# Kernel optimization log

Measured on AMD Instinct MI355X. Metric: run time of the kernel, lower is better.

Reference implementation:

```python
import jax, jax.numpy as jnp
import numpy as np

VTH = 1.0
DECAY = 0.25


def setup_inputs() -> dict:
    key = jax.random.key(0)
    x = jax.random.normal(key, (32, 64, 16384), dtype=jnp.float32)
    return {"x": x}


def reference(x):
    # x: [T, B, N]; sequential leaky-integrate-fire over T with hard reset.
    def step(mem, xt):
        mem = mem * DECAY + xt
        out_s = (mem > VTH).astype(mem.dtype)
        out_bp = jnp.clip(mem, VTH - 1.0, VTH + 1.0) * 0.5  # surrogate
        # forward value = out_s (0/1), gradient flows through out_bp
        out_i = jax.lax.stop_gradient(out_s - out_bp) + out_bp
        mem = mem * (1.0 - out_i)  # reset=True branch
        return mem, out_i

    mem0 = jnp.zeros_like(x[0])
    _, out = jax.lax.scan(step, mem0, x)
    return out
```

## Files before the change

kernel.cpp:

```cpp
#include <hip/hip_runtime.h>


typedef float f32x2 __attribute__((ext_vector_type(2)));

__global__ __launch_bounds__(256) void lif_fwd_kernel(
    const f32x2* __restrict__ x, f32x2* __restrict__ out, int BN2, int T) {
    const int i = blockIdx.x * blockDim.x + threadIdx.x;
    if (i >= BN2) return;

    const f32x2* xp = x + i;
    f32x2* op = out + i;

    float mx = 0.f, my = 0.f;

    #pragma unroll 32
    for (int t = 0; t < T; ++t) {
        const f32x2 xt = xp[(size_t)t * (size_t)BN2];

        f32x2 s;
        mx = mx * 0.25f + xt.x;
        my = my * 0.25f + xt.y;

        s.x = (mx > 1.0f) ? 1.0f : 0.0f;
        s.y = (my > 1.0f) ? 1.0f : 0.0f;

        mx = (s.x != 0.0f) ? 0.0f : mx;
        my = (s.y != 0.0f) ? 0.0f : my;

        op[(size_t)t * (size_t)BN2] = s;
    }
}

extern "C" void kernel_launch(void* const* d_in, const int* in_sizes, int n_in,
                              void* d_out, int out_size, void* d_ws, size_t ws_size,
                              hipStream_t stream) {
    const float* x = (const float*)d_in[0];
    float* out = (float*)d_out;

    const int T = 32;
    const int total = in_sizes[0];
    const int BN = total / T;
    const int BN2 = BN / 2;

    const int block = 256;
    const int grid = (BN2 + block - 1) / block;

    lif_fwd_kernel<<<grid, block, 0, stream>>>(
        (const f32x2*)x, (f32x2*)out, BN2, T);
}
```

Before: 45.49 us.

## Prefetch all timesteps into registers with scalar per-thread elements

Each thread now handles one float instead of a float2 pair and loads all 32 timesteps into registers before running the sequential recurrence. Issuing every load up front is meant to expose memory-level parallelism and hide latency, and doubling the thread count raises occupancy. The occupancy hint of 8 blocks per CU and the removed bounds check assume BN divides evenly by 256. The exchange is narrower 4-byte accesses and 32 live registers per thread.

After: 51.54 us. 1.13x slower.

```diff
diff --git a/kernel.cpp b/kernel.cpp
--- a/kernel.cpp
+++ b/kernel.cpp
@@ -1,33 +1,22 @@
 #include <hip/hip_runtime.h>
 
 
-typedef float f32x2 __attribute__((ext_vector_type(2)));
+__global__ __launch_bounds__(256, 8) void lif_fwd_kernel(
+    const float* __restrict__ x, float* __restrict__ out, int BN) {
+    const size_t i = (size_t)blockIdx.x * 256 + threadIdx.x;
 
-__global__ __launch_bounds__(256) void lif_fwd_kernel(
-    const f32x2* __restrict__ x, f32x2* __restrict__ out, int BN2, int T) {
-    const int i = blockIdx.x * blockDim.x + threadIdx.x;
-    if (i >= BN2) return;
+    float xv[32];
+    #pragma unroll
+    for (int t = 0; t < 32; ++t)
+        xv[t] = x[(size_t)t * BN + i];
 
-    const f32x2* xp = x + i;
-    f32x2* op = out + i;
-
-    float mx = 0.f, my = 0.f;
-
-    #pragma unroll 32
-    for (int t = 0; t < T; ++t) {
-        const f32x2 xt = xp[(size_t)t * (size_t)BN2];
-
-        f32x2 s;
-        mx = mx * 0.25f + xt.x;
-        my = my * 0.25f + xt.y;
-
-        s.x = (mx > 1.0f) ? 1.0f : 0.0f;
-        s.y = (my > 1.0f) ? 1.0f : 0.0f;
-
-        mx = (s.x != 0.0f) ? 0.0f : mx;
-        my = (s.y != 0.0f) ? 0.0f : my;
-
-        op[(size_t)t * (size_t)BN2] = s;
+    float mem = 0.f;
+    #pragma unroll
+    for (int t = 0; t < 32; ++t) {
+        mem = mem * 0.25f + xv[t];
+        const float s = (mem > 1.0f) ? 1.0f : 0.0f;
+        mem = (s != 0.0f) ? 0.0f : mem;
+        out[(size_t)t * BN + i] = s;
     }
 }
 
@@ -40,11 +29,9 @@
     const int T = 32;
     const int total = in_sizes[0];
     const int BN = total / T;
-    const int BN2 = BN / 2;
 
     const int block = 256;
-    const int grid = (BN2 + block - 1) / block;
+    const int grid = BN / block;
 
-    lif_fwd_kernel<<<grid, block, 0, stream>>>(
-        (const f32x2*)x, (f32x2*)out, BN2, T);
+    lif_fwd_kernel<<<grid, block, 0, stream>>>(x, out, BN);
 }
```
